# Optimization experiments

Measured on AMD Instinct MI355X. Metric: run time of the kernel, lower is better.

Reference implementation:

```python
import jax, jax.numpy as jnp
import numpy as np

N, E = 50000, 800000
DIN, DOUT, DEDGE, HEADS = 128, 128, 64, 1


def setup_inputs() -> dict:
    key = jax.random.key(0)
    ks = jax.random.split(key, 16)
    s = 0.02
    inp = {
        "x": jax.random.normal(ks[0], (N, DIN), jnp.float32),
        "edge_index": jax.random.randint(ks[1], (2, E), 0, N, dtype=jnp.int32),
        "edge_attr": jax.random.normal(ks[2], (E, DEDGE), jnp.float32),
        # TransformerConv params (PyG defaults: q/k/v/skip have bias, lin_edge has no bias)
        "Wq": jax.random.normal(ks[3], (DIN, HEADS * DOUT), jnp.float32) * s,
        "bq": jnp.zeros((HEADS * DOUT,), jnp.float32),
        "Wk": jax.random.normal(ks[4], (DIN, HEADS * DOUT), jnp.float32) * s,
        "bk": jnp.zeros((HEADS * DOUT,), jnp.float32),
        "Wv": jax.random.normal(ks[5], (DIN, HEADS * DOUT), jnp.float32) * s,
        "bv": jnp.zeros((HEADS * DOUT,), jnp.float32),
        "We": jax.random.normal(ks[6], (DEDGE, HEADS * DOUT), jnp.float32) * s,
        "Wskip": jax.random.normal(ks[7], (DIN, HEADS * DOUT), jnp.float32) * s,
        "bskip": jnp.zeros((HEADS * DOUT,), jnp.float32),
        # LayerNorm
        "ln_g": jnp.ones((DOUT,), jnp.float32),
        "ln_b": jnp.zeros((DOUT,), jnp.float32),
        # GatedResidualConnection
        "Wres": jax.random.normal(ks[8], (DIN, DOUT), jnp.float32) * s,
        "bres": jnp.zeros((DOUT,), jnp.float32),
        "Wgate": jax.random.normal(ks[9], (DIN, 1), jnp.float32) * s,
        "bgate": jnp.zeros((1,), jnp.float32),
    }
    return inp


def _transformer_conv(x, edge_index, edge_attr, Wq, bq, Wk, bk, Wv, bv, We, Wskip, bskip):
    H, C = HEADS, DOUT
    src, dst = edge_index[0], edge_index[1]  # j -> i (aggregate at dst)
    q = (x @ Wq + bq).reshape(-1, H, C)
    k = (x @ Wk + bk).reshape(-1, H, C)
    v = (x @ Wv + bv).reshape(-1, H, C)
    e = (edge_attr @ We).reshape(-1, H, C)  # [E,H,C]
    k_j = k[src] + e
    v_j = v[src] + e
    q_i = q[dst]
    alpha = jnp.sum(q_i * k_j, axis=-1) / jnp.sqrt(jnp.float32(C))  # [E,H]
    # segment softmax over incoming edges of each dst node
    amax = jax.ops.segment_max(alpha, dst, num_segments=N)  # [N,H]
    ex = jnp.exp(alpha - amax[dst])
    denom = jax.ops.segment_sum(ex, dst, num_segments=N)  # [N,H]
    p = ex / denom[dst]  # [E,H]
    out = jax.ops.segment_sum(p[..., None] * v_j, dst, num_segments=N)  # [N,H,C]
    out = out.reshape(-1, H * C)
    out = out + (x @ Wskip + bskip)  # root weight skip
    return out


def reference(x, edge_index, edge_attr, Wq, bq, Wk, bk, Wv, bv, We, Wskip, bskip,
              ln_g, ln_b, Wres, bres, Wgate, bgate):
    out = _transformer_conv(x, edge_index, edge_attr, Wq, bq, Wk, bk, Wv, bv, We, Wskip, bskip)
    # LayerNorm(out_channels)
    mu = jnp.mean(out, axis=-1, keepdims=True)
    var = jnp.mean(jnp.square(out - mu), axis=-1, keepdims=True)
    out = (out - mu) / jnp.sqrt(var + 1e-5) * ln_g + ln_b
    out = jax.nn.relu(out)
    # gated residual
    residual = x @ Wres + bres
    gate = jax.nn.sigmoid(x @ Wgate + bgate)  # [N,1]
    return gate * out + (1.0 - gate) * residual
```

## Files before the change

### kernel.cpp

```cpp
#include <hip/hip_runtime.h>
#include <math.h>

#define NN 50000
#define EE 800000
#define NPAD 50048
#define PC 768

typedef short bf16x8 __attribute__((ext_vector_type(8)));
typedef float f32x4 __attribute__((ext_vector_type(4)));

#define ASCALE 0.08838834764831845f

__device__ inline unsigned short f2bf(float f)
{
    unsigned u = __float_as_uint(f);
    u = u + 0x7fff + ((u >> 16) & 1);
    return (unsigned short)(u >> 16);
}

__device__ inline float bfu(unsigned short us)
{
    return __uint_as_float((unsigned)us << 16);
}

__global__ __launch_bounds__(256) void k_wprep(const float* __restrict__ Wq,
                                               const float* __restrict__ bq,
                                               const float* __restrict__ We,
                                               float* __restrict__ wqe,
                                               float* __restrict__ bqe)
{
    int idx = blockIdx.x * 256 + threadIdx.x;
    if (idx < 8192) {
        int r = idx >> 6, m = idx & 63;
        float acc = 0.f;
        for (int c = 0; c < 128; ++c) acc += Wq[r * 128 + c] * We[m * 128 + c];
        wqe[r * 64 + m] = acc;
    } else if (idx < 8256) {
        int m = idx - 8192;
        float acc = 0.f;
        for (int c = 0; c < 128; ++c) acc += bq[c] * We[m * 128 + c];
        bqe[m] = acc;
    }
}

__global__ __launch_bounds__(256) void k_packx(const float* __restrict__ x,
                                               short* __restrict__ Xb)
{
    int t = blockIdx.x * 256 + threadIdx.x;
    int base = t * 4;
    if (base >= NPAD * 128) return;
    short s0 = 0, s1 = 0, s2 = 0, s3 = 0;
    if (base < NN * 128) {
        const float4 v = *(const float4*)(x + base);
        s0 = f2bf(v.x); s1 = f2bf(v.y); s2 = f2bf(v.z); s3 = f2bf(v.w);
    }
    short4 o; o.x = s0; o.y = s1; o.z = s2; o.w = s3;
    *(short4*)(Xb + base) = o;
}

__global__ __launch_bounds__(256) void k_packw(
    const float* __restrict__ Wq, const float* __restrict__ bq,
    const float* __restrict__ Wk, const float* __restrict__ bk,
    const float* __restrict__ Wv, const float* __restrict__ bv,
    const float* __restrict__ Wskip, const float* __restrict__ bskip,
    const float* __restrict__ Wres, const float* __restrict__ bres,
    const float* __restrict__ Wgate, const float* __restrict__ bgate,
    const float* __restrict__ wqe, const float* __restrict__ bqe,
    const float* __restrict__ We,
    short* __restrict__ WT, float* __restrict__ bias,
    unsigned short* __restrict__ WeTb)
{
    int idx = blockIdx.x * 256 + threadIdx.x;
    if (idx < PC * 128) {
        int col = idx >> 7, k = idx & 127;
        float v;
        if (col < 128)      v = Wq[k * 128 + col];
        else if (col < 256) v = Wk[k * 128 + (col - 128)];
        else if (col < 384) v = Wv[k * 128 + (col - 256)];
        else if (col < 512) v = Wskip[k * 128 + (col - 384)];
        else if (col < 640) v = Wres[k * 128 + (col - 512)];
        else if (col < 704) v = wqe[k * 64 + (col - 640)];
        else if (col == 704) v = Wgate[k];
        else                v = 0.f;
        WT[col * 128 + k] = (short)f2bf(v);
    } else if (idx < PC * 128 + PC) {
        int col = idx - PC * 128;
        float b;
        if (col < 128)      b = bq[col];
        else if (col < 256) b = bk[col - 128];
        else if (col < 384) b = bv[col - 256];
        else if (col < 512) b = bskip[col - 384];
        else if (col < 640) b = bres[col - 512];
        else if (col < 704) b = bqe[col - 640];
        else if (col == 704) b = bgate[0];
        else                b = 0.f;
        bias[col] = b;
    } else if (idx < PC * 128 + PC + 128 * 72) {
        int i2 = idx - (PC * 128 + PC);
        int c = i2 / 72, kk = i2 % 72;
        WeTb[i2] = (kk < 64) ? f2bf(We[kk * 128 + c]) : (unsigned short)0;
    }
}

#define LROW 136
__global__ __launch_bounds__(256) void k_gemm(const short* __restrict__ Xb,
                                              const short* __restrict__ WT,
                                              const float* __restrict__ bias,
                                              float* __restrict__ Pq,
                                              unsigned short* __restrict__ Pe,
                                              unsigned short* __restrict__ KVb16)
{
    __shared__ short Al[128 * LROW];
    __shared__ short Bl[64 * LROW];

    int bn = blockIdx.x;
    int bm = blockIdx.y;
    int tid = threadIdx.x;

    const short* gA = Xb + (size_t)bm * 128 * 128;
    const short* gB = WT + (size_t)bn * 64 * 128;

#pragma unroll
    for (int it = 0; it < 8; ++it) {
        int g = it * 256 + tid;
        int row = g >> 4, c8 = g & 15;
        *(bf16x8*)&Al[row * LROW + c8 * 8] = *(const bf16x8*)(gA + g * 8);
    }
#pragma unroll
    for (int it = 0; it < 4; ++it) {
        int g = it * 256 + tid;
        int row = g >> 4, c8 = g & 15;
        *(bf16x8*)&Bl[row * LROW + c8 * 8] = *(const bf16x8*)(gB + g * 8);
    }
    __syncthreads();

    int wave = tid >> 6, lane = tid & 63;
    int quad = lane >> 4, l16 = lane & 15;
    int r0 = wave * 32;

    f32x4 acc[2][4] = {};
#pragma unroll
    for (int ks = 0; ks < 4; ++ks) {
        int k0 = ks * 32 + quad * 8;
        bf16x8 af0 = *(const bf16x8*)&Al[(r0 + l16) * LROW + k0];
        bf16x8 af1 = *(const bf16x8*)&Al[(r0 + 16 + l16) * LROW + k0];
#pragma unroll
        for (int cn = 0; cn < 4; ++cn) {
            bf16x8 bfr = *(const bf16x8*)&Bl[(cn * 16 + l16) * LROW + k0];
            acc[0][cn] = __builtin_amdgcn_mfma_f32_16x16x32_bf16(af0, bfr, acc[0][cn], 0, 0, 0);
            acc[1][cn] = __builtin_amdgcn_mfma_f32_16x16x32_bf16(af1, bfr, acc[1][cn], 0, 0, 0);
        }
    }

    bool isKV = (bn >= 2 && bn <= 5);
#pragma unroll
    for (int half = 0; half < 2; ++half) {
        int growb = bm * 128 + r0 + half * 16 + quad * 4;
#pragma unroll
        for (int cn = 0; cn < 4; ++cn) {
            int gcol = bn * 64 + cn * 16 + l16;
            float b = bias[gcol];
#pragma unroll
            for (int i = 0; i < 4; ++i) {
                int grow = growb + i;
                if (grow < NN) {
                    float v = acc[half][cn][i] + b;
                    if (bn < 2) {
                        Pq[(size_t)grow * 128 + gcol] = v;
                    } else if (isKV) {
                        int c, sub;
                        if (gcol < 192)      { c = gcol - 128; sub = 0; }
                        else if (gcol < 256) { c = gcol - 192; sub = 1; }
                        else if (gcol < 320) { c = gcol - 256; sub = 2; }
                        else                 { c = gcol - 320; sub = 3; }
                        KVb16[(size_t)grow * 256 + c * 4 + sub] = f2bf(v);
                    } else if (gcol <= 704) {
                        if (gcol == 704) v = 1.f / (1.f + __expf(-v));
                        Pe[(size_t)grow * 384 + (gcol - 384)] = f2bf(v);
                    }
                }
            }
        }
    }
}

__global__ __launch_bounds__(256) void k_hist(const int* __restrict__ ei,
                                              int* __restrict__ deg, int E)
{
    int e = blockIdx.x * 256 + threadIdx.x;
    if (e < E) atomicAdd(&deg[ei[E + e]], 1);
}

__global__ __launch_bounds__(256) void k_scan1(const int* __restrict__ deg,
                                               int* __restrict__ rs,
                                               int* __restrict__ cs, int n)
{
    __shared__ int sh[256];
    int base = blockIdx.x * 1024;
    int t = threadIdx.x;
    int idx = base + t * 4;
    int v[4];
#pragma unroll
    for (int k = 0; k < 4; ++k) v[k] = (idx + k < n) ? deg[idx + k] : 0;
    int sum = v[0] + v[1] + v[2] + v[3];
    sh[t] = sum;
    __syncthreads();
    for (int off = 1; off < 256; off <<= 1) {
        int add = (t >= off) ? sh[t - off] : 0;
        __syncthreads();
        sh[t] += add;
        __syncthreads();
    }
    int run = sh[t] - sum;
    if (t == 255) cs[blockIdx.x] = sh[255];
#pragma unroll
    for (int k = 0; k < 4; ++k) {
        if (idx + k < n) rs[idx + k] = run;
        run += v[k];
    }
}

__global__ void k_scan2(int* __restrict__ cs, int nc)
{
    __shared__ int sh[64];
    int t = threadIdx.x;
    sh[t] = (t < nc) ? cs[t] : 0;
    __syncthreads();
    if (t == 0) {
        int acc = 0;
        for (int i = 0; i < nc; ++i) { int v = sh[i]; sh[i] = acc; acc += v; }
    }
    __syncthreads();
    if (t < nc) cs[t] = sh[t];
}

__global__ __launch_bounds__(256) void k_scan3(int* __restrict__ rs,
                                               const int* __restrict__ cs,
                                               int* __restrict__ cur, int n, int E)
{
    int i = blockIdx.x * 256 + threadIdx.x;
    if (i < n) {
        int v = rs[i] + cs[i >> 10];
        rs[i] = v;
        cur[i] = v;
    } else if (i == n) {
        rs[n] = E;
    }
}

__global__ __launch_bounds__(256) void k_scatter(const int* __restrict__ ei,
                                                 int* __restrict__ cur,
                                                 int2* __restrict__ sj, int E)
{
    int e = blockIdx.x * 256 + threadIdx.x;
    if (e < E) {
        int d = ei[E + e];
        int pos = atomicAdd(&cur[d], 1);
        int2 v; v.x = ei[e]; v.y = e;
        sj[pos] = v;
    }
}

__global__ __launch_bounds__(256) void k_attn_fused(
    const float* __restrict__ Pq, const unsigned short* __restrict__ Pe,
    const unsigned int* __restrict__ KVb,
    const float* __restrict__ ea, const unsigned short* __restrict__ WeTb,
    const int* __restrict__ rs, const int2* __restrict__ sj,
    const float* __restrict__ ln_g, const float* __restrict__ ln_b,
    float* __restrict__ out)
{
    __shared__ unsigned short Sb_l[4 * 64];
    __shared__ float att_l[4 * 128];

    int tid = threadIdx.x;
    int wave = tid >> 6, lane = tid & 63;
    int node = blockIdx.x * 4 + wave;

    const float* Qrow = Pq + (size_t)node * 128;
    const unsigned short* Erow = Pe + (size_t)node * 384;
    float q0 = Qrow[lane];
    float q1 = Qrow[64 + lane];
    float wq = bfu(Erow[256 + lane]);

    float accd = 0.f, t0 = 0.f, t1 = 0.f, sA = 0.f;
    int beg = rs[node], end = rs[node + 1];

    int p = beg;
    for (; p + 8 <= end; p += 8) {
        float pp[8], aa[8], v0[8], v1[8];
#pragma unroll
        for (int u = 0; u < 8; ++u) {
            long long sv = __builtin_nontemporal_load((const long long*)(sj + p + u));
            int sx = (int)sv, sy = (int)(sv >> 32);
            uint2 kv2 = *(const uint2*)(KVb + (size_t)sx * 128 + 2 * lane);
            float a = __builtin_nontemporal_load(ea + (size_t)sy * 64 + lane);
            float k0 = __uint_as_float(kv2.x << 16);
            float k1 = __uint_as_float(kv2.x & 0xffff0000u);
            v0[u] = __uint_as_float(kv2.y << 16);
            v1[u] = __uint_as_float(kv2.y & 0xffff0000u);
            aa[u] = a;
            pp[u] = q0 * k0 + q1 * k1 + wq * a;
        }
#pragma unroll
        for (int o = 32; o > 0; o >>= 1) {
#pragma unroll
            for (int u = 0; u < 8; ++u) pp[u] += __shfl_xor(pp[u], o);
        }
#pragma unroll
        for (int u = 0; u < 8; ++u) {
            float ex = __expf(pp[u] * ASCALE);
            accd += ex;
            t0 += ex * v0[u];
            t1 += ex * v1[u];
            sA += ex * aa[u];
        }
    }
    for (; p + 4 <= end; p += 4) {
        float pp[4], aa[4], v0[4], v1[4];
#pragma unroll
        for (int u = 0; u < 4; ++u) {
            long long sv = __builtin_nontemporal_load((const long long*)(sj + p + u));
            int sx = (int)sv, sy = (int)(sv >> 32);
            uint2 kv2 = *(const uint2*)(KVb + (size_t)sx * 128 + 2 * lane);
            float a = __builtin_nontemporal_load(ea + (size_t)sy * 64 + lane);
            float k0 = __uint_as_float(kv2.x << 16);
            float k1 = __uint_as_float(kv2.x & 0xffff0000u);
            v0[u] = __uint_as_float(kv2.y << 16);
            v1[u] = __uint_as_float(kv2.y & 0xffff0000u);
            aa[u] = a;
            pp[u] = q0 * k0 + q1 * k1 + wq * a;
        }
#pragma unroll
        for (int o = 32; o > 0; o >>= 1) {
#pragma unroll
            for (int u = 0; u < 4; ++u) pp[u] += __shfl_xor(pp[u], o);
        }
#pragma unroll
        for (int u = 0; u < 4; ++u) {
            float ex = __expf(pp[u] * ASCALE);
            accd += ex;
            t0 += ex * v0[u];
            t1 += ex * v1[u];
            sA += ex * aa[u];
        }
    }
    for (; p < end; ++p) {
        long long sv = __builtin_nontemporal_load((const long long*)(sj + p));
        int sx = (int)sv, sy = (int)(sv >> 32);
        uint2 kv2 = *(const uint2*)(KVb + (size_t)sx * 128 + 2 * lane);
        float a = __builtin_nontemporal_load(ea + (size_t)sy * 64 + lane);
        float k0 = __uint_as_float(kv2.x << 16);
        float k1 = __uint_as_float(kv2.x & 0xffff0000u);
        float vv0 = __uint_as_float(kv2.y << 16);
        float vv1 = __uint_as_float(kv2.y & 0xffff0000u);
        float part = q0 * k0 + q1 * k1 + wq * a;
#pragma unroll
        for (int o = 32; o > 0; o >>= 1) part += __shfl_xor(part, o);
        float ex = __expf(part * ASCALE);
        accd += ex;
        t0 += ex * vv0;
        t1 += ex * vv1;
        sA += ex * a;
    }


    Sb_l[wave * 64 + lane] = f2bf(sA);
    __syncthreads();

    {
        int quad = lane >> 4, l16 = lane & 15;
        int arow = l16 & 3;
        bf16x8 a0 = *(const bf16x8*)&Sb_l[arow * 64 + quad * 8];
        bf16x8 a1 = *(const bf16x8*)&Sb_l[arow * 64 + 32 + quad * 8];
#pragma unroll
        for (int c2 = 0; c2 < 2; ++c2) {
            int cn = wave * 2 + c2;
            int r = cn * 16 + l16;
            bf16x8 b0 = *(const bf16x8*)(WeTb + r * 72 + quad * 8);
            bf16x8 b1 = *(const bf16x8*)(WeTb + r * 72 + 32 + quad * 8);
            f32x4 acc = {};
            acc = __builtin_amdgcn_mfma_f32_16x16x32_bf16(a0, b0, acc, 0, 0, 0);
            acc = __builtin_amdgcn_mfma_f32_16x16x32_bf16(a1, b1, acc, 0, 0, 0);
            if (quad == 0) {
#pragma unroll
                for (int i = 0; i < 4; ++i)
                    att_l[i * 128 + cn * 16 + l16] = acc[i];
            }
        }
    }
    __syncthreads();

    float rcp = accd > 0.f ? 1.f / accd : 0.f;
    float a0f = (t0 + att_l[wave * 128 + lane]) * rcp + bfu(Erow[lane]);
    float a1f = (t1 + att_l[wave * 128 + 64 + lane]) * rcp + bfu(Erow[64 + lane]);

    float s = a0f + a1f;
#pragma unroll
    for (int o = 32; o > 0; o >>= 1) s += __shfl_xor(s, o);
    float mean = s * (1.f / 128.f);
    float d0 = a0f - mean, d1 = a1f - mean;
    float vs = d0 * d0 + d1 * d1;
#pragma unroll
    for (int o = 32; o > 0; o >>= 1) vs += __shfl_xor(vs, o);
    float inv = rsqrtf(vs * (1.f / 128.f) + 1e-5f);
    float n0 = d0 * inv * ln_g[lane] + ln_b[lane];
    float n1 = d1 * inv * ln_g[64 + lane] + ln_b[64 + lane];
    n0 = fmaxf(n0, 0.f);
    n1 = fmaxf(n1, 0.f);

    float g = bfu(Erow[320]);
    float r0 = bfu(Erow[128 + lane]);
    float r1 = bfu(Erow[192 + lane]);
    out[(size_t)node * 128 + lane] = g * n0 + (1.f - g) * r0;
    out[(size_t)node * 128 + 64 + lane] = g * n1 + (1.f - g) * r1;
}

extern "C" void kernel_launch(void* const* d_in, const int* in_sizes, int n_in,
                              void* d_out, int out_size, void* d_ws, size_t ws_size,
                              hipStream_t stream)
{
    const float* x     = (const float*)d_in[0];
    const int*   ei    = (const int*)d_in[1];
    const float* ea    = (const float*)d_in[2];
    const float* Wq    = (const float*)d_in[3];
    const float* bq    = (const float*)d_in[4];
    const float* Wk    = (const float*)d_in[5];
    const float* bk    = (const float*)d_in[6];
    const float* Wv    = (const float*)d_in[7];
    const float* bv    = (const float*)d_in[8];
    const float* We    = (const float*)d_in[9];
    const float* Wskip = (const float*)d_in[10];
    const float* bskip = (const float*)d_in[11];
    const float* ln_g  = (const float*)d_in[12];
    const float* ln_b  = (const float*)d_in[13];
    const float* Wres  = (const float*)d_in[14];
    const float* bres  = (const float*)d_in[15];
    const float* Wgate = (const float*)d_in[16];
    const float* bgate = (const float*)d_in[17];
    float* out = (float*)d_out;

    float* W = (float*)d_ws;
    size_t o = 0;
    auto falloc = [&](size_t e) { size_t r = o; o += e; return r; };
    size_t oPQ   = falloc((size_t)NN * 128);
    size_t oWQE  = falloc(8192);
    size_t oBQE  = falloc(64);
    size_t oBIAS = falloc(PC);
    size_t oKVB  = falloc((size_t)NN * 128);

    short* SB = (short*)(W + o);
    size_t oXB  = 0;
    size_t oWT  = oXB + (size_t)NPAD * 128;
    size_t oWET = oWT + (size_t)PC * 128;
    size_t oPE  = oWET + 128 * 72;
    size_t sh_total = oPE + (size_t)NN * 384;

    int* IB = (int*)(SB + ((sh_total + 1) & ~(size_t)1));
    size_t io = 0;
    auto ialloc = [&](size_t e) { size_t r = io; io += e; return r; };
    size_t oSJ   = ialloc((size_t)2 * EE);
    size_t oDEG  = ialloc(NN);
    size_t oRS   = ialloc(NN + 1);
    size_t oCUR  = ialloc(NN);
    size_t oCS   = ialloc(64);

    hipMemsetAsync(IB + oDEG, 0, NN * sizeof(int), stream);

    k_wprep<<<33, 256, 0, stream>>>(Wq, bq, We, W + oWQE, W + oBQE);
    k_packx<<<(NPAD * 128 / 4 + 255) / 256, 256, 0, stream>>>(x, SB + oXB);
    k_packw<<<(PC * 128 + PC + 128 * 72 + 255) / 256, 256, 0, stream>>>(
        Wq, bq, Wk, bk, Wv, bv, Wskip, bskip, Wres, bres, Wgate, bgate,
        W + oWQE, W + oBQE, We, SB + oWT, W + oBIAS,
        (unsigned short*)(SB + oWET));

    dim3 ggrid(PC / 64, NPAD / 128);
    k_gemm<<<ggrid, 256, 0, stream>>>(SB + oXB, SB + oWT, W + oBIAS, W + oPQ,
                                      (unsigned short*)(SB + oPE),
                                      (unsigned short*)(W + oKVB));

    k_hist<<<(EE + 255) / 256, 256, 0, stream>>>(ei, IB + oDEG, EE);
    k_scan1<<<49, 256, 0, stream>>>(IB + oDEG, IB + oRS, IB + oCS, NN);
    k_scan2<<<1, 64, 0, stream>>>(IB + oCS, 49);
    k_scan3<<<(NN + 256) / 256, 256, 0, stream>>>(IB + oRS, IB + oCS, IB + oCUR, NN, EE);
    k_scatter<<<(EE + 255) / 256, 256, 0, stream>>>(ei, IB + oCUR, (int2*)(IB + oSJ), EE);

    k_attn_fused<<<NN / 4, 256, 0, stream>>>(
        W + oPQ, (const unsigned short*)(SB + oPE),
        (const unsigned int*)(W + oKVB), ea,
        (const unsigned short*)(SB + oWET),
        IB + oRS, (const int2*)(IB + oSJ), ln_g, ln_b, out);
}
```

Measured before the change: 578.2 us.

## Swap MFMA operands for row-contiguous vector epilogue stores; merge prep kernels

Swaps the A/B operands of the MFMA so each lane holds four consecutive output columns for one row. The GEMM epilogue can then write float4 and packed bf16x4 stores instead of scattered scalar ones. The K/V weight columns are permuted during packing so the interleaved KV layout comes out contiguous. The x-pack and Wq·We precompute kernels are merged into one launch to save a kernel launch. The sigmoid gate check now only applies to the first element of a 4-column group, which is correct only because column 704 is 4-aligned.

```diff
diff --git a/kernel.cpp b/kernel.cpp
--- a/kernel.cpp
+++ b/kernel.cpp
@@ -23,39 +23,39 @@
     return __uint_as_float((unsigned)us << 16);
 }
 
-__global__ __launch_bounds__(256) void k_wprep(const float* __restrict__ Wq,
-                                               const float* __restrict__ bq,
-                                               const float* __restrict__ We,
-                                               float* __restrict__ wqe,
-                                               float* __restrict__ bqe)
-{
-    int idx = blockIdx.x * 256 + threadIdx.x;
-    if (idx < 8192) {
-        int r = idx >> 6, m = idx & 63;
-        float acc = 0.f;
-        for (int c = 0; c < 128; ++c) acc += Wq[r * 128 + c] * We[m * 128 + c];
-        wqe[r * 64 + m] = acc;
-    } else if (idx < 8256) {
-        int m = idx - 8192;
-        float acc = 0.f;
-        for (int c = 0; c < 128; ++c) acc += bq[c] * We[m * 128 + c];
-        bqe[m] = acc;
-    }
-}
-
-__global__ __launch_bounds__(256) void k_packx(const float* __restrict__ x,
-                                               short* __restrict__ Xb)
-{
-    int t = blockIdx.x * 256 + threadIdx.x;
-    int base = t * 4;
-    if (base >= NPAD * 128) return;
-    short s0 = 0, s1 = 0, s2 = 0, s3 = 0;
-    if (base < NN * 128) {
-        const float4 v = *(const float4*)(x + base);
-        s0 = f2bf(v.x); s1 = f2bf(v.y); s2 = f2bf(v.z); s3 = f2bf(v.w);
-    }
-    short4 o; o.x = s0; o.y = s1; o.z = s2; o.w = s3;
-    *(short4*)(Xb + base) = o;
+#define NXB (NPAD * 128 / 4 / 256)
+__global__ __launch_bounds__(256) void k_prep(const float* __restrict__ x,
+                                              short* __restrict__ Xb,
+                                              const float* __restrict__ Wq,
+                                              const float* __restrict__ bq,
+                                              const float* __restrict__ We,
+                                              float* __restrict__ wqe,
+                                              float* __restrict__ bqe)
+{
+    if (blockIdx.x < NXB) {
+        int t = blockIdx.x * 256 + threadIdx.x;
+        int base = t * 4;
+        short s0 = 0, s1 = 0, s2 = 0, s3 = 0;
+        if (base < NN * 128) {
+            const float4 v = *(const float4*)(x + base);
+            s0 = f2bf(v.x); s1 = f2bf(v.y); s2 = f2bf(v.z); s3 = f2bf(v.w);
+        }
+        short4 o; o.x = s0; o.y = s1; o.z = s2; o.w = s3;
+        *(short4*)(Xb + base) = o;
+    } else {
+        int idx = (blockIdx.x - NXB) * 256 + threadIdx.x;
+        if (idx < 8192) {
+            int r = idx >> 6, m = idx & 63;
+            float acc = 0.f;
+            for (int c = 0; c < 128; ++c) acc += Wq[r * 128 + c] * We[m * 128 + c];
+            wqe[r * 64 + m] = acc;
+        } else if (idx < 8256) {
+            int m = idx - 8192;
+            float acc = 0.f;
+            for (int c = 0; c < 128; ++c) acc += bq[c] * We[m * 128 + c];
+            bqe[m] = acc;
+        }
+    }
 }
 
 __global__ __launch_bounds__(256) void k_packw(
@@ -75,8 +75,11 @@
         int col = idx >> 7, k = idx & 127;
         float v;
         if (col < 128)      v = Wq[k * 128 + col];
-        else if (col < 256) v = Wk[k * 128 + (col - 128)];
-        else if (col < 384) v = Wv[k * 128 + (col - 256)];
+        else if (col < 384) {
+            int t = col - 128, c = t >> 2, s = t & 3;
+            v = (s == 0) ? Wk[k * 128 + c] : (s == 1) ? Wk[k * 128 + c + 64]
+              : (s == 2) ? Wv[k * 128 + c] : Wv[k * 128 + c + 64];
+        }
         else if (col < 512) v = Wskip[k * 128 + (col - 384)];
         else if (col < 640) v = Wres[k * 128 + (col - 512)];
         else if (col < 704) v = wqe[k * 64 + (col - 640)];
@@ -87,8 +90,11 @@
         int col = idx - PC * 128;
         float b;
         if (col < 128)      b = bq[col];
-        else if (col < 256) b = bk[col - 128];
-        else if (col < 384) b = bv[col - 256];
+        else if (col < 384) {
+            int t = col - 128, c = t >> 2, s = t & 3;
+            b = (s == 0) ? bk[c] : (s == 1) ? bk[c + 64]
+              : (s == 2) ? bv[c] : bv[c + 64];
+        }
         else if (col < 512) b = bskip[col - 384];
         else if (col < 640) b = bres[col - 512];
         else if (col < 704) b = bqe[col - 640];
@@ -147,37 +153,38 @@
 #pragma unroll
         for (int cn = 0; cn < 4; ++cn) {
             bf16x8 bfr = *(const bf16x8*)&Bl[(cn * 16 + l16) * LROW + k0];
-            acc[0][cn] = __builtin_amdgcn_mfma_f32_16x16x32_bf16(af0, bfr, acc[0][cn], 0, 0, 0);
-            acc[1][cn] = __builtin_amdgcn_mfma_f32_16x16x32_bf16(af1, bfr, acc[1][cn], 0, 0, 0);
+            acc[0][cn] = __builtin_amdgcn_mfma_f32_16x16x32_bf16(bfr, af0, acc[0][cn], 0, 0, 0);
+            acc[1][cn] = __builtin_amdgcn_mfma_f32_16x16x32_bf16(bfr, af1, acc[1][cn], 0, 0, 0);
         }
     }
 
     bool isKV = (bn >= 2 && bn <= 5);
 #pragma unroll
     for (int half = 0; half < 2; ++half) {
-        int growb = bm * 128 + r0 + half * 16 + quad * 4;
-#pragma unroll
-        for (int cn = 0; cn < 4; ++cn) {
-            int gcol = bn * 64 + cn * 16 + l16;
-            float b = bias[gcol];
-#pragma unroll
-            for (int i = 0; i < 4; ++i) {
-                int grow = growb + i;
-                if (grow < NN) {
-                    float v = acc[half][cn][i] + b;
-                    if (bn < 2) {
-                        Pq[(size_t)grow * 128 + gcol] = v;
-                    } else if (isKV) {
-                        int c, sub;
-                        if (gcol < 192)      { c = gcol - 128; sub = 0; }
-                        else if (gcol < 256) { c = gcol - 192; sub = 1; }
-                        else if (gcol < 320) { c = gcol - 256; sub = 2; }
-                        else                 { c = gcol - 320; sub = 3; }
-                        KVb16[(size_t)grow * 256 + c * 4 + sub] = f2bf(v);
-                    } else if (gcol <= 704) {
-                        if (gcol == 704) v = 1.f / (1.f + __expf(-v));
-                        Pe[(size_t)grow * 384 + (gcol - 384)] = f2bf(v);
-                    }
+        int grow = bm * 128 + r0 + half * 16 + l16;
+        if (grow < NN) {
+#pragma unroll
+            for (int cn = 0; cn < 4; ++cn) {
+                int colbase = bn * 64 + cn * 16 + quad * 4;
+                const float4 b4 = *(const float4*)(bias + colbase);
+                float v0 = acc[half][cn][0] + b4.x;
+                float v1 = acc[half][cn][1] + b4.y;
+                float v2 = acc[half][cn][2] + b4.z;
+                float v3 = acc[half][cn][3] + b4.w;
+                if (bn < 2) {
+                    float4 o; o.x = v0; o.y = v1; o.z = v2; o.w = v3;
+                    *(float4*)(Pq + (size_t)grow * 128 + colbase) = o;
+                } else if (isKV) {
+                    uint2 o;
+                    o.x = (unsigned)f2bf(v0) | ((unsigned)f2bf(v1) << 16);
+                    o.y = (unsigned)f2bf(v2) | ((unsigned)f2bf(v3) << 16);
+                    *(uint2*)(KVb16 + (size_t)grow * 256 + (colbase - 128)) = o;
+                } else {
+                    if (colbase == 704) v0 = 1.f / (1.f + __expf(-v0));
+                    uint2 o;
+                    o.x = (unsigned)f2bf(v0) | ((unsigned)f2bf(v1) << 16);
+                    o.y = (unsigned)f2bf(v2) | ((unsigned)f2bf(v3) << 16);
+                    *(uint2*)(Pe + (size_t)grow * 384 + (colbase - 384)) = o;
                 }
             }
         }
@@ -466,8 +473,8 @@
 
     hipMemsetAsync(IB + oDEG, 0, NN * sizeof(int), stream);
 
-    k_wprep<<<33, 256, 0, stream>>>(Wq, bq, We, W + oWQE, W + oBQE);
-    k_packx<<<(NPAD * 128 / 4 + 255) / 256, 256, 0, stream>>>(x, SB + oXB);
+    k_prep<<<NXB + 33, 256, 0, stream>>>(x, SB + oXB, Wq, bq, We,
+                                         W + oWQE, W + oBQE);
     k_packw<<<(PC * 128 + PC + 128 * 72 + 255) / 256, 256, 0, stream>>>(
         Wq, bq, Wk, bk, Wv, bv, Wskip, bskip, Wres, bres, Wgate, bgate,
         W + oWQE, W + oBQE, We, SB + oWT, W + oBIAS,
```

After: 547.7 us. -5.3%, faster.
